# Kernel optimization log

Hardware: AMD Instinct MI355X
Metric: run time of the kernel (lower is better)

## Reference

```python
import jax, jax.numpy as jnp
import numpy as np

EMBED_DIM = 1024
NUM_HEADS = 16
ROTARY_THETA = 10000.0


def _rotate_half(t):
    d = t.shape[-1] // 2
    t1, t2 = t[..., :d], t[..., d:]
    return jnp.concatenate([-t2, t1], axis=-1)


def _rope_cos_sin(seq_len, head_dim, dtype):
    # inv_freq over even indices, standard RoPE
    inv_freq = 1.0 / (ROTARY_THETA ** (jnp.arange(0, head_dim, 2, dtype=jnp.float32) / head_dim))
    freqs = jnp.arange(seq_len, dtype=jnp.float32)[:, None] * inv_freq[None, :]  # (S, D/2)
    emb = jnp.concatenate([freqs, freqs], axis=-1)  # (S, D)
    # broadcast over (b, s, h, d)
    return jnp.cos(emb).astype(dtype)[None, :, None, :], jnp.sin(emb).astype(dtype)[None, :, None, :]


def setup_inputs() -> dict:
    key = jax.random.key(0)
    ks = jax.random.split(key, 4)
    B, S, E = 2, 2048, EMBED_DIM
    scale = 1.0 / np.sqrt(E)
    return {
        "x": jax.random.normal(ks[0], (B, S, E), dtype=jnp.float32),
        "attention_mask": jnp.zeros((B, 1, 1, S), dtype=jnp.float32),
        "Wq": jax.random.normal(ks[1], (E, E), dtype=jnp.float32) * scale,
        "bq": jnp.zeros((E,), dtype=jnp.float32),
        "Wk": jax.random.normal(ks[2], (E, E), dtype=jnp.float32) * scale,
        "bk": jnp.zeros((E,), dtype=jnp.float32),
        "Wv": jax.random.normal(ks[3], (E, E), dtype=jnp.float32) * scale,
        "bv": jnp.zeros((E,), dtype=jnp.float32),
    }


def reference(x, attention_mask, Wq, bq, Wk, bk, Wv, bv):
    B, S, E = x.shape
    H = NUM_HEADS
    D = E // H

    q = (x @ Wq + bq).reshape(B, S, H, D)
    k = (x @ Wk + bk).reshape(B, S, H, D)
    v = (x @ Wv + bv).reshape(B, S, H, D)

    cos, sin = _rope_cos_sin(S, D, q.dtype)
    q = q * cos + _rotate_half(q) * sin
    k = k * cos + _rotate_half(k) * sin

    # attention_mask: additive padding bias (b,1,1,k) broadcast over heads & queries
    scores = jnp.einsum("bqhd,bkhd->bhqk", q, k) / jnp.sqrt(jnp.asarray(D, dtype=q.dtype))
    scores = scores + attention_mask  # broadcasts to (b,h,q,k)
    attn = jax.nn.softmax(scores, axis=-1)
    out = jnp.einsum("bhqk,bkhd->bqhd", attn, v)
    return out.reshape(B, S, E)
```

## Files before the change

kernel.cpp:

```cpp
#include <hip/hip_runtime.h>

typedef __attribute__((ext_vector_type(8)))  short bf16x8;
typedef __attribute__((ext_vector_type(4)))  short s16x4;
typedef __attribute__((ext_vector_type(4)))  float f32x4;
typedef __attribute__((ext_vector_type(16))) float f32x16;
typedef __attribute__((ext_vector_type(4)))  unsigned u32x4;
typedef __attribute__((ext_vector_type(4)))  _Float16 f16x4;

#define B_  2
#define S_  2048
#define H_  16
#define D_  64
#define E_  1024
#define M_  (B_*S_)
#define L2E 1.44269504f

__device__ __forceinline__ unsigned short f2bf(float f){
  unsigned x = __builtin_bit_cast(unsigned, f);
  x += 0x7fffu + ((x >> 16) & 1u);
  return (unsigned short)(x >> 16);
}
__device__ __forceinline__ unsigned pk_bf16(float lo, float hi){
  unsigned short a = __builtin_bit_cast(unsigned short, (__bf16)lo);
  unsigned short b = __builtin_bit_cast(unsigned short, (__bf16)hi);
  return (unsigned)a | ((unsigned)b << 16);
}

#define GLD16(gp, lp) __builtin_amdgcn_global_load_lds( \
    (const __attribute__((address_space(1))) unsigned*)(gp), \
    (__attribute__((address_space(3))) unsigned*)(lp), 16, 0, 0)

__global__ __launch_bounds__(256) void k_cvt(const float* __restrict__ in, short* __restrict__ out,
                                             const float* __restrict__ mask,
                                             float* ct, float* st, float* maskC){
  int i = blockIdx.x*256 + threadIdx.x;
  if(i < S_*32){
    int s = i >> 5, f = i & 31;
    float invf = powf(10000.0f, -(float)f / 32.0f);
    float ph = (float)s * invf;
    ct[i] = cosf(ph);
    st[i] = sinf(ph);
    if(i < B_*S_) maskC[i] = fmaf(mask[i], L2E, -17.0f);
  }
  int j = i*4;
  float4 v = *(const float4*)(in + j);
  s16x4 o = { (short)f2bf(v.x), (short)f2bf(v.y), (short)f2bf(v.z), (short)f2bf(v.w) };
  *(s16x4*)(out + j) = o;
}

__global__ __launch_bounds__(256) void k_wt(const float* __restrict__ Wq, const float* __restrict__ Wk,
                                            const float* __restrict__ Wv, short* __restrict__ wt){
  const float* W = blockIdx.z==0 ? Wq : (blockIdx.z==1 ? Wk : Wv);
  short* out = wt + (size_t)blockIdx.z*E_*E_;
  __shared__ short tile[64][72];
  int nb = blockIdx.x*64, kb = blockIdx.y*64;
  int t = threadIdx.x;
  {
    int r = t>>2, c0 = (t&3)*16;
    const float* src = W + (size_t)(kb+r)*E_ + nb + c0;
    #pragma unroll
    for(int i=0;i<4;i++){
      float4 v = *(const float4*)(src + i*4);
      tile[r][c0+i*4+0] = (short)f2bf(v.x);
      tile[r][c0+i*4+1] = (short)f2bf(v.y);
      tile[r][c0+i*4+2] = (short)f2bf(v.z);
      tile[r][c0+i*4+3] = (short)f2bf(v.w);
    }
  }
  __syncthreads();
  {
    int n = t>>2, k0 = (t&3)*16;
    short* dst = out + (size_t)(nb+n)*E_ + kb + k0;
    bf16x8 o0, o1;
    #pragma unroll
    for(int i=0;i<8;i++){ o0[i] = tile[k0+i][n]; o1[i] = tile[k0+8+i][n]; }
    *(bf16x8*)dst = o0;
    *(bf16x8*)(dst+8) = o1;
  }
}

__global__ __launch_bounds__(256) void k_gemm(const short* __restrict__ A, const short* __restrict__ WT,
                                              const float* __restrict__ biasq, const float* __restrict__ biask,
                                              const float* __restrict__ biasv,
                                              short* __restrict__ oq, short* __restrict__ ok, short* __restrict__ ovt,
                                              const float* __restrict__ cost, const float* __restrict__ sint){
  const int z = blockIdx.z;
  const short* Bw = WT + (size_t)z*E_*E_;
  const float* bias = z==0 ? biasq : (z==1 ? biask : biasv);
  __shared__ short As[128*32];
  __shared__ short Bs[128*32];
  const int t = threadIdx.x, lane = t & 63, wid = t >> 6;
  const int mb = blockIdx.x*128, nb = blockIdx.y*128;
  const int wm = (wid>>1)*64, wn = (wid&1)*64;
  f32x4 acc[4][4] = {};
  for(int kt=0; kt<E_/32; kt++){
    __syncthreads();
    {
      int f0 = t, f1 = t + 256;
      GLD16(A  + (size_t)(mb + (f0>>2))*E_ + kt*32 + (f0&3)*8, &As[f0*8]);
      GLD16(A  + (size_t)(mb + (f1>>2))*E_ + kt*32 + (f1&3)*8, &As[f1*8]);
      GLD16(Bw + (size_t)(nb + (f0>>2))*E_ + kt*32 + (f0&3)*8, &Bs[f0*8]);
      GLD16(Bw + (size_t)(nb + (f1>>2))*E_ + kt*32 + (f1&3)*8, &Bs[f1*8]);
    }
    __syncthreads();
    bf16x8 af[4], bfv[4];
    #pragma unroll
    for(int mf=0; mf<4; mf++)
      af[mf] = *(const bf16x8*)&As[(wm + mf*16 + (lane&15))*32 + (lane>>4)*8];
    #pragma unroll
    for(int nf=0; nf<4; nf++)
      bfv[nf] = *(const bf16x8*)&Bs[(wn + nf*16 + (lane&15))*32 + (lane>>4)*8];
    #pragma unroll
    for(int mf=0; mf<4; mf++)
      #pragma unroll
      for(int nf=0; nf<4; nf++)
        acc[mf][nf] = __builtin_amdgcn_mfma_f32_16x16x32_bf16(af[mf], bfv[nf], acc[mf][nf], 0, 0, 0);
  }
  const int col16 = lane & 15, rg = lane >> 4;
  float bvs[4];
  #pragma unroll
  for(int nf=0; nf<4; nf++) bvs[nf] = bias[nb + wn + nf*16 + col16];
  if(z == 2){
    #pragma unroll
    for(int mf=0; mf<4; mf++){
      int row0 = mb + wm + mf*16 + rg*4;
      int bb2 = row0 >> 11, ss = row0 & (S_-1);
      #pragma unroll
      for(int nf=0; nf<4; nf++){
        int e = nb + wn + nf*16 + col16;
        int hh = e >> 6, dd = e & 63;
        s16x4 w = { (short)f2bf(acc[mf][nf][0]+bvs[nf]), (short)f2bf(acc[mf][nf][1]+bvs[nf]),
                    (short)f2bf(acc[mf][nf][2]+bvs[nf]), (short)f2bf(acc[mf][nf][3]+bvs[nf]) };
        *(s16x4*)(ovt + ((size_t)(bb2*H_+hh)*D_+dd)*S_ + ss) = w;
      }
    }
  } else {
    short* out = (z==0) ? oq : ok;
    const float qs = (z==0) ? (0.125f*L2E) : 1.0f;
    #pragma unroll
    for(int mf=0; mf<4; mf++)
      #pragma unroll
      for(int r=0; r<4; r++){
        int row = mb + wm + mf*16 + rg*4 + r;
        int srow = row & (S_-1);
        const float* cb = cost + (size_t)srow*32;
        const float* sb = sint + (size_t)srow*32;
        #pragma unroll
        for(int nf=0; nf<2; nf++){
          int d = nf*16 + col16;
          float c = cb[d], sn = sb[d];
          float x0 = acc[mf][nf][r]   + bvs[nf];
          float x1 = acc[mf][nf+2][r] + bvs[nf+2];
          out[(size_t)row*E_ + nb + wn + nf*16 + col16]     = (short)f2bf((x0*c - x1*sn)*qs);
          out[(size_t)row*E_ + nb + wn + (nf+2)*16 + col16] = (short)f2bf((x1*c + x0*sn)*qs);
        }
      }
  }
}

__global__ __launch_bounds__(256,4) void k_attn(
    const short* __restrict__ qg, const short* __restrict__ kg,
    const short* __restrict__ vtg, const float* __restrict__ maskC,
    float* __restrict__ o0g, _Float16* __restrict__ o1g, float* __restrict__ lpart){
  __shared__ short Ks[2][64*72];
  __shared__ short Vs[2][64*72];
  const int flat = blockIdx.x;
  const int v = flat >> 3;
  const int bh = (flat & 7)*4 + (v >> 5);
  const int inner = v & 31;
  const int qb = inner >> 1, sp = inner & 1;
  const int h = bh & 15, b = bh >> 4;
  const int tid = threadIdx.x, wid = tid>>6, lane = tid&63;
  const int l31 = lane & 31, hl = lane >> 5;
  const int qw = qb*128 + wid*32;
  const int rr = tid>>3, ch = tid&7;
  const int kb0 = sp*16;
  const int NT = 16;

  bf16x8 qf[4];
  {
    const short* qp = qg + ((size_t)(b*S_ + qw + l31)*H_ + h)*D_;
    #pragma unroll
    for(int dk=0; dk<4; dk++)
      qf[dk] = *(const bf16x8*)(qp + dk*16 + hl*8);
  }
  f32x16 O0 = {}, O1 = {};
  float l_run = 0.f;
  const float* mrow = maskC + (size_t)b*S_;

  bf16x8 ka, kc, va, vc;
#define LOADT(kb) { \
    const short* ks_ = kg + ((size_t)(b*S_ + (kb)*64 + rr)*H_ + h)*D_ + ch*8; \
    ka = *(const bf16x8*)ks_;  kc = *(const bf16x8*)(ks_ + 32*H_*D_); \
    const short* vs_ = vtg + ((size_t)(b*H_ + h)*D_ + rr)*S_ + (kb)*64 + ch*8; \
    va = *(const bf16x8*)vs_;  vc = *(const bf16x8*)(vs_ + 32*S_); }
#define WRITET(pp) { \
    *(bf16x8*)&Ks[pp][rr*72 + ch*8]      = ka; \
    *(bf16x8*)&Ks[pp][(rr+32)*72 + ch*8] = kc; \
    *(bf16x8*)&Vs[pp][rr*72 + ch*8]      = va; \
    *(bf16x8*)&Vs[pp][(rr+32)*72 + ch*8] = vc; }

  LOADT(kb0);
  WRITET(0);
  LOADT(kb0+1);
  __syncthreads();

  int p = 0;
  for(int tt=0; tt<NT; tt++){
    f32x16 s0 = {}, s1 = {};
    __builtin_amdgcn_s_setprio(1);
    #pragma unroll
    for(int dk=0; dk<4; dk++){
      bf16x8 kf0 = *(const bf16x8*)&Ks[p][(l31)*72 + dk*16 + hl*8];
      bf16x8 kf1 = *(const bf16x8*)&Ks[p][(32+l31)*72 + dk*16 + hl*8];
      s0 = __builtin_amdgcn_mfma_f32_32x32x16_bf16(kf0, qf[dk], s0, 0,0,0);
      s1 = __builtin_amdgcn_mfma_f32_32x32x16_bf16(kf1, qf[dk], s1, 0,0,0);
    }
    __builtin_amdgcn_s_setprio(0);
    {
      const float* mt = mrow + (kb0+tt)*64 + hl*4;
      #pragma unroll
      for(int bb=0; bb<4; bb++){
        f32x4 mv0 = *(const f32x4*)(mt + bb*8);
        f32x4 mv1 = *(const f32x4*)(mt + 32 + bb*8);
        #pragma unroll
        for(int a=0; a<4; a++){ s0[bb*4+a] += mv0[a]; s1[bb*4+a] += mv1[a]; }
      }
    }
    #pragma unroll
    for(int i=0;i<16;i++) s0[i] = __builtin_amdgcn_exp2f(s0[i]);
    #pragma unroll
    for(int i=0;i<16;i++) s1[i] = __builtin_amdgcn_exp2f(s1[i]);
    float la=0.f, lb=0.f, lc=0.f, ld=0.f;
    #pragma unroll
    for(int i=0;i<4;i++){
      la += s0[i];   lb += s0[4+i];  lc += s0[8+i];  ld += s0[12+i];
      la += s1[i];   lb += s1[4+i];  lc += s1[8+i];  ld += s1[12+i];
    }
    float ls = (la+lb)+(lc+ld);
    ls += __shfl_xor(ls, 32);
    l_run += ls;

    unsigned w0a[8], w1a[8];
    #pragma unroll
    for(int c=0;c<8;c++){
      int base = (c&3)*4;
      float p0 = (c & 4) ? s1[base+0] : s0[base+0];
      float p1 = (c & 4) ? s1[base+1] : s0[base+1];
      float p2 = (c & 4) ? s1[base+2] : s0[base+2];
      float p3 = (c & 4) ? s1[base+3] : s0[base+3];
      w0a[c] = pk_bf16(p0, p1);
      w1a[c] = pk_bf16(p2, p3);
    }

    if(tt+1 < NT){
      WRITET(p^1);
      if(tt+2 < NT) LOADT(kb0+tt+2);
    }

    __builtin_amdgcn_s_setprio(1);
    #pragma unroll
    for(int ksl=0; ksl<4; ksl++){
      unsigned a0 = w0a[2*ksl], b0 = w0a[2*ksl+1];
      unsigned a1 = w1a[2*ksl], b1 = w1a[2*ksl+1];
      asm("v_permlane32_swap_b32 %0, %1" : "+v"(a0), "+v"(b0));
      asm("v_permlane32_swap_b32 %0, %1" : "+v"(a1), "+v"(b1));
      u32x4 pw = { a0, a1, b0, b1 };
      bf16x8 pf = __builtin_bit_cast(bf16x8, pw);
      bf16x8 vf0 = *(const bf16x8*)&Vs[p][(l31)*72 + ksl*16 + hl*8];
      bf16x8 vf1 = *(const bf16x8*)&Vs[p][(32+l31)*72 + ksl*16 + hl*8];
      O0 = __builtin_amdgcn_mfma_f32_32x32x16_bf16(pf, vf0, O0, 0,0,0);
      O1 = __builtin_amdgcn_mfma_f32_32x32x16_bf16(pf, vf1, O1, 0,0,0);
    }
    __builtin_amdgcn_s_setprio(0);
    __syncthreads();
    p ^= 1;
  }
#undef LOADT
#undef WRITET

  if(sp == 0){
    #pragma unroll
    for(int bb=0; bb<4; bb++)
      #pragma unroll
      for(int a=0; a<4; a++){
        int qrow = qw + a + 8*bb + 4*hl;
        float* op = o0g + ((size_t)(b*S_ + qrow)*H_ + h)*D_;
        op[l31]      = O0[bb*4+a];
        op[32 + l31] = O1[bb*4+a];
      }
  } else {
    #pragma unroll
    for(int bb=0; bb<4; bb++)
      #pragma unroll
      for(int a=0; a<4; a++){
        int qrow = qw + a + 8*bb + 4*hl;
        _Float16* op = o1g + ((size_t)(b*S_ + qrow)*H_ + h)*D_;
        op[l31]      = (_Float16)O0[bb*4+a];
        op[32 + l31] = (_Float16)O1[bb*4+a];
      }
  }
  if(lane < 32)
    lpart[(size_t)sp*(M_*H_) + (size_t)(b*S_ + qw + l31)*H_ + h] = l_run;
}

__global__ __launch_bounds__(256) void k_comb(float* __restrict__ out, const _Float16* __restrict__ o1,
                                              const float* __restrict__ lpart){
  int i = blockIdx.x*256 + threadIdx.x;
  int idx = i*4;
  int lidx = idx >> 6;
  float linv = 1.f / (lpart[lidx] + lpart[M_*H_ + lidx]);
  f32x4 a = *(f32x4*)(out + idx);
  f16x4 bb = *(const f16x4*)(o1 + idx);
  f32x4 r = { (a[0] + (float)bb[0])*linv, (a[1] + (float)bb[1])*linv,
              (a[2] + (float)bb[2])*linv, (a[3] + (float)bb[3])*linv };
  *(f32x4*)(out + idx) = r;
}

extern "C" void kernel_launch(void* const* d_in, const int* in_sizes, int n_in,
                              void* d_out, int out_size, void* d_ws, size_t ws_size,
                              hipStream_t stream){
  (void)in_sizes; (void)n_in; (void)out_size; (void)ws_size;
  const float* x    = (const float*)d_in[0];
  const float* mask = (const float*)d_in[1];
  const float* Wq   = (const float*)d_in[2];
  const float* bq   = (const float*)d_in[3];
  const float* Wk   = (const float*)d_in[4];
  const float* bk   = (const float*)d_in[5];
  const float* Wv   = (const float*)d_in[6];
  const float* bv   = (const float*)d_in[7];
  float* out = (float*)d_out;
  char* ws = (char*)d_ws;
  float* cost  = (float*)(ws);
  float* sint  = (float*)(ws + (256u<<10));
  float* maskC = (float*)(ws + (512u<<10));
  float* lpart = (float*)(ws + (768u<<10));
  short* xb    = (short*)(ws + (2u<<20));
  short* wt    = (short*)(ws + (10u<<20));
  short* qb    = (short*)(ws + (16u<<20));
  short* kb    = (short*)(ws + (24u<<20));
  short* vtb   = (short*)(ws + (32u<<20));
  _Float16* o1 = (_Float16*)xb;

  k_cvt<<<dim3(4096), dim3(256), 0, stream>>>(x, xb, mask, cost, sint, maskC);
  k_wt<<<dim3(16,16,3), dim3(256), 0, stream>>>(Wq, Wk, Wv, wt);
  k_gemm<<<dim3(32,8,3), dim3(256), 0, stream>>>(xb, wt, bq, bk, bv, qb, kb, vtb, cost, sint);
  k_attn<<<dim3(1024), dim3(256), 0, stream>>>(qb, kb, vtb, maskC, out, o1, lpart);
  k_comb<<<dim3(4096), dim3(256), 0, stream>>>(out, o1, lpart);
}
```

Measured before the change: 118.1 us.

## Single-buffer K/V tiles, stage mask in LDS, compute row sums via MFMA

Replaces the double-buffered K/V LDS tiles with single buffers refilled after a barrier, adding a second sync per iteration. It stages the mask slice in shared memory and uses it as the initial accumulator of the QK MFMA, so the separate add pass goes away. It also replaces the scalar row-sum reduction and cross-lane shuffle with an extra MFMA against a ones vector. The aim is to cut VALU work and LDS footprint, possibly for occupancy, at the cost of less overlap between loads and compute, an extra barrier, and sums taken from bf16-rounded probabilities.

```diff
diff --git a/kernel.cpp b/kernel.cpp
--- a/kernel.cpp
+++ b/kernel.cpp
@@ -162,8 +162,9 @@
     const short* __restrict__ qg, const short* __restrict__ kg,
     const short* __restrict__ vtg, const float* __restrict__ maskC,
     float* __restrict__ o0g, _Float16* __restrict__ o1g, float* __restrict__ lpart){
-  __shared__ short Ks[2][64*72];
-  __shared__ short Vs[2][64*72];
+  __shared__ short Ks[64*72];
+  __shared__ short Vs[64*72];
+  __shared__ float Mh[1024];
   const int flat = blockIdx.x;
   const int v = flat >> 3;
   const int bh = (flat & 7)*4 + (v >> 5);
@@ -184,9 +185,9 @@
     for(int dk=0; dk<4; dk++)
       qf[dk] = *(const bf16x8*)(qp + dk*16 + hl*8);
   }
-  f32x16 O0 = {}, O1 = {};
-  float l_run = 0.f;
-  const float* mrow = maskC + (size_t)b*S_;
+  const short one_bf = (short)0x3F80;
+  const bf16x8 vones = { one_bf,one_bf,one_bf,one_bf,one_bf,one_bf,one_bf,one_bf };
+  f32x16 O0 = {}, O1 = {}, l_acc = {};
 
   bf16x8 ka, kc, va, vc;
 #define LOADT(kb) { \
@@ -194,52 +195,44 @@
     ka = *(const bf16x8*)ks_;  kc = *(const bf16x8*)(ks_ + 32*H_*D_); \
     const short* vs_ = vtg + ((size_t)(b*H_ + h)*D_ + rr)*S_ + (kb)*64 + ch*8; \
     va = *(const bf16x8*)vs_;  vc = *(const bf16x8*)(vs_ + 32*S_); }
-#define WRITET(pp) { \
-    *(bf16x8*)&Ks[pp][rr*72 + ch*8]      = ka; \
-    *(bf16x8*)&Ks[pp][(rr+32)*72 + ch*8] = kc; \
-    *(bf16x8*)&Vs[pp][rr*72 + ch*8]      = va; \
-    *(bf16x8*)&Vs[pp][(rr+32)*72 + ch*8] = vc; }
-
+#define WRITET() { \
+    *(bf16x8*)&Ks[rr*72 + ch*8]      = ka; \
+    *(bf16x8*)&Ks[(rr+32)*72 + ch*8] = kc; \
+    *(bf16x8*)&Vs[rr*72 + ch*8]      = va; \
+    *(bf16x8*)&Vs[(rr+32)*72 + ch*8] = vc; }
+
+  *(f32x4*)&Mh[tid*4] = *(const f32x4*)(maskC + (size_t)b*S_ + kb0*64 + tid*4);
   LOADT(kb0);
-  WRITET(0);
-  LOADT(kb0+1);
+  WRITET();
   __syncthreads();
 
-  int p = 0;
   for(int tt=0; tt<NT; tt++){
-    f32x16 s0 = {}, s1 = {};
+    if(tt+1 < NT) LOADT(kb0+tt+1);
+
+    f32x16 s0, s1;
+    {
+      const int mbase = tt*64 + hl*4;
+      #pragma unroll
+      for(int bb=0; bb<4; bb++){
+        f32x4 mv0 = *(const f32x4*)&Mh[mbase + bb*8];
+        f32x4 mv1 = *(const f32x4*)&Mh[mbase + 32 + bb*8];
+        #pragma unroll
+        for(int a=0; a<4; a++){ s0[bb*4+a] = mv0[a]; s1[bb*4+a] = mv1[a]; }
+      }
+    }
     __builtin_amdgcn_s_setprio(1);
     #pragma unroll
     for(int dk=0; dk<4; dk++){
-      bf16x8 kf0 = *(const bf16x8*)&Ks[p][(l31)*72 + dk*16 + hl*8];
-      bf16x8 kf1 = *(const bf16x8*)&Ks[p][(32+l31)*72 + dk*16 + hl*8];
+      bf16x8 kf0 = *(const bf16x8*)&Ks[(l31)*72 + dk*16 + hl*8];
+      bf16x8 kf1 = *(const bf16x8*)&Ks[(32+l31)*72 + dk*16 + hl*8];
       s0 = __builtin_amdgcn_mfma_f32_32x32x16_bf16(kf0, qf[dk], s0, 0,0,0);
       s1 = __builtin_amdgcn_mfma_f32_32x32x16_bf16(kf1, qf[dk], s1, 0,0,0);
     }
     __builtin_amdgcn_s_setprio(0);
-    {
-      const float* mt = mrow + (kb0+tt)*64 + hl*4;
-      #pragma unroll
-      for(int bb=0; bb<4; bb++){
-        f32x4 mv0 = *(const f32x4*)(mt + bb*8);
-        f32x4 mv1 = *(const f32x4*)(mt + 32 + bb*8);
-        #pragma unroll
-        for(int a=0; a<4; a++){ s0[bb*4+a] += mv0[a]; s1[bb*4+a] += mv1[a]; }
-      }
-    }
     #pragma unroll
     for(int i=0;i<16;i++) s0[i] = __builtin_amdgcn_exp2f(s0[i]);
     #pragma unroll
     for(int i=0;i<16;i++) s1[i] = __builtin_amdgcn_exp2f(s1[i]);
-    float la=0.f, lb=0.f, lc=0.f, ld=0.f;
-    #pragma unroll
-    for(int i=0;i<4;i++){
-      la += s0[i];   lb += s0[4+i];  lc += s0[8+i];  ld += s0[12+i];
-      la += s1[i];   lb += s1[4+i];  lc += s1[8+i];  ld += s1[12+i];
-    }
-    float ls = (la+lb)+(lc+ld);
-    ls += __shfl_xor(ls, 32);
-    l_run += ls;
 
     unsigned w0a[8], w1a[8];
     #pragma unroll
@@ -253,11 +246,6 @@
       w1a[c] = pk_bf16(p2, p3);
     }
 
-    if(tt+1 < NT){
-      WRITET(p^1);
-      if(tt+2 < NT) LOADT(kb0+tt+2);
-    }
-
     __builtin_amdgcn_s_setprio(1);
     #pragma unroll
     for(int ksl=0; ksl<4; ksl++){
@@ -267,14 +255,19 @@
       asm("v_permlane32_swap_b32 %0, %1" : "+v"(a1), "+v"(b1));
       u32x4 pw = { a0, a1, b0, b1 };
       bf16x8 pf = __builtin_bit_cast(bf16x8, pw);
-      bf16x8 vf0 = *(const bf16x8*)&Vs[p][(l31)*72 + ksl*16 + hl*8];
-      bf16x8 vf1 = *(const bf16x8*)&Vs[p][(32+l31)*72 + ksl*16 + hl*8];
-      O0 = __builtin_amdgcn_mfma_f32_32x32x16_bf16(pf, vf0, O0, 0,0,0);
-      O1 = __builtin_amdgcn_mfma_f32_32x32x16_bf16(pf, vf1, O1, 0,0,0);
+      bf16x8 vf0 = *(const bf16x8*)&Vs[(l31)*72 + ksl*16 + hl*8];
+      bf16x8 vf1 = *(const bf16x8*)&Vs[(32+l31)*72 + ksl*16 + hl*8];
+      O0    = __builtin_amdgcn_mfma_f32_32x32x16_bf16(pf, vf0, O0, 0,0,0);
+      O1    = __builtin_amdgcn_mfma_f32_32x32x16_bf16(pf, vf1, O1, 0,0,0);
+      l_acc = __builtin_amdgcn_mfma_f32_32x32x16_bf16(pf, vones, l_acc, 0,0,0);
     }
     __builtin_amdgcn_s_setprio(0);
+
     __syncthreads();
-    p ^= 1;
+    if(tt+1 < NT){
+      WRITET();
+      __syncthreads();
+    }
   }
 #undef LOADT
 #undef WRITET
@@ -300,8 +293,13 @@
         op[32 + l31] = (_Float16)O1[bb*4+a];
       }
   }
-  if(lane < 32)
-    lpart[(size_t)sp*(M_*H_) + (size_t)(b*S_ + qw + l31)*H_ + h] = l_run;
+  if(l31 == 0){
+    #pragma unroll
+    for(int r=0; r<16; r++){
+      int qrow = qw + (r&3) + 8*(r>>2) + 4*hl;
+      lpart[(size_t)sp*(M_*H_) + (size_t)(b*S_ + qrow)*H_ + h] = l_acc[r];
+    }
+  }
 }
 
 __global__ __launch_bounds__(256) void k_comb(float* __restrict__ out, const _Float16* __restrict__ o1,
```

Measured after the change: 155.9 us. 1.32x slower.
